# Performance work log

Measured on AMD Instinct MI355X. Metric: run time of the kernel, lower is better.

## Reference

```python
import jax, jax.numpy as jnp
import numpy as np

N, E = 10000, 160000
D, H, C, FF, L = 128, 4, 32, 512, 2
INNER = H * C
VOCAB, RELVOCAB = 32000, 100
EPS = 1e-6
GATE_BIAS = 3.0


def _layer_norm(x, w, b):
    mu = jnp.mean(x, axis=-1, keepdims=True)
    var = jnp.mean(jnp.square(x - mu), axis=-1, keepdims=True)
    return (x - mu) * jax.lax.rsqrt(var + EPS) * w + b


def setup_inputs() -> dict:
    key = jax.random.key(0)
    ks = jax.random.split(key, 24)
    s = 1.0 / np.sqrt(D)
    inp = {
        "node_ids": jax.random.randint(ks[0], (N,), 0, VOCAB),
        "edge_index": jax.random.randint(ks[1], (2, E), 0, N),
        "edge_ids": jax.random.randint(ks[2], (E,), 0, RELVOCAB),
        "node_emb": jax.random.normal(ks[3], (VOCAB, D), jnp.float32),
        "edge_emb": jax.random.normal(ks[4], (RELVOCAB, D), jnp.float32),
        # per-layer stacked params (torch Linear weight layout [out, in])
        "ln_w": jnp.ones((L, D), jnp.float32),
        "ln_b": jnp.zeros((L, D), jnp.float32),
        "q_w": jax.random.normal(ks[5], (L, INNER, D), jnp.float32) * (1.0 / np.sqrt(D * C)),
        "relA_w": jax.random.normal(ks[6], (L, FF, 2 * D), jnp.float32) * s,
        "relA_b": jnp.zeros((L, FF), jnp.float32),
        "relB_w": jax.random.normal(ks[7], (L, D, FF), jnp.float32) * s,
        "relB_b": jnp.zeros((L, D), jnp.float32),
        "relG_w": jax.random.normal(ks[8], (L, D, FF), jnp.float32) * s,
        "relG_b": jnp.zeros((L, D), jnp.float32),
        "k_w": jax.random.normal(ks[9], (L, INNER, 2 * D), jnp.float32) * s,
        "v_w": jax.random.normal(ks[10], (L, INNER, D), jnp.float32) * s,
        "o_w": jax.random.normal(ks[11], (L, D, INNER), jnp.float32) * (1.0 / np.sqrt(INNER)),
        "ff_ln_w": jnp.ones((L, D), jnp.float32),
        "ff_ln_b": jnp.zeros((L, D), jnp.float32),
        "wi_w": jax.random.normal(ks[12], (L, FF, D), jnp.float32) * s,
        "wo_w": jax.random.normal(ks[13], (L, D, FF), jnp.float32) * (1.0 / np.sqrt(FF)),
    }
    return inp


def _forward(node_ids, edge_index, edge_ids, node_emb, edge_emb, ln_w, ln_b,
             q_w, relA_w, relA_b, relB_w, relB_b, relG_w, relG_b,
             k_w, v_w, o_w, ff_ln_w, ff_ln_b, wi_w, wo_w):
    x = node_emb[node_ids]          # [N, D]
    ef = edge_emb[edge_ids]         # [E, D]
    src = edge_index[0]             # j (source / kv side)
    dst = edge_index[1]             # i (target / query side)
    for l in range(L):
        # --- relational self-attention ---
        q = _layer_norm(x, ln_w[l], ln_b[l])
        q = (q @ q_w[l].T).reshape(N, H, C)
        kv_j = x[src]                                   # [E, D]
        cat = jnp.concatenate([kv_j, ef], axis=-1)      # [E, 2D]
        inter = jax.nn.celu(cat @ relA_w[l].T + relA_b[l])   # [E, FF]
        gate = jax.nn.sigmoid(inter @ relG_w[l].T + relG_b[l] + GATE_BIAS)
        k_add = inter @ relB_w[l].T + relB_b[l]
        kv2 = kv_j * gate + k_add * (1.0 - gate)        # [E, D]
        k = (jnp.concatenate([kv2, ef], axis=-1) @ k_w[l].T).reshape(E, H, C)
        v = (kv2 @ v_w[l].T).reshape(E, H, C)
        scores = jnp.sum(q[dst] * k, axis=-1)           # [E, H]
        smax = jax.ops.segment_max(scores, dst, num_segments=N)
        ex = jnp.exp(scores - smax[dst])
        denom = jax.ops.segment_sum(ex, dst, num_segments=N)
        alpha = ex / denom[dst]                         # [E, H]
        msg = (v * alpha[..., None]).reshape(E, INNER)
        agg = jax.ops.segment_sum(msg, dst, num_segments=N)  # [N, INNER]
        x = x + agg @ o_w[l].T
        # --- feed-forward (T5-style, pre-LN, relu, residual) ---
        h = _layer_norm(x, ff_ln_w[l], ff_ln_b[l])
        x = x + jax.nn.relu(h @ wi_w[l].T) @ wo_w[l].T
    return x


def reference(node_ids, edge_index, edge_ids, node_emb, edge_emb, ln_w, ln_b,
              q_w, relA_w, relA_b, relB_w, relB_b, relG_w, relG_b,
              k_w, v_w, o_w, ff_ln_w, ff_ln_b, wi_w, wo_w):
    return _forward(node_ids, edge_index, edge_ids, node_emb, edge_emb, ln_w, ln_b,
                    q_w, relA_w, relA_b, relB_w, relB_b, relG_w, relG_b,
                    k_w, v_w, o_w, ff_ln_w, ff_ln_b, wi_w, wo_w)
```

## Files before the change

### kernel.cpp

```cpp
#include <hip/hip_runtime.h>
#include <hip/hip_bf16.h>

#define NN 10000
#define EE 160000
#define DD 128
#define HH 4
#define CC 32
#define FFF 512
#define LL 2
#define RELV 100
#define EPS 1e-6f
#define GATE_BIAS 3.0f
#define BM 64
#define NT 16

typedef __bf16 bf16x8 __attribute__((ext_vector_type(8)));
typedef float f32x4 __attribute__((ext_vector_type(4)));
typedef float f32x16 __attribute__((ext_vector_type(16)));

#define MFMA(a,b,c)   __builtin_amdgcn_mfma_f32_16x16x32_bf16((a),(b),(c),0,0,0)
#define MFMA32(a,b,c) __builtin_amdgcn_mfma_f32_32x32x16_bf16((a),(b),(c),0,0,0)

__device__ __forceinline__ int swzK(int e, int b){ return e*256 + (b ^ ((e&7)<<4)); }
__device__ __forceinline__ int swz128(int e, int b){ return e*256 + (b ^ ((e&7)<<4)); }
__device__ __forceinline__ int swz512(int e, int b){ return e*1024 + (b ^ ((e&7)<<4)); }

__global__ __launch_bounds__(128) void k_gx(
    const int* __restrict__ node_ids, const float* __restrict__ node_emb,
    float* __restrict__ x, ushort* __restrict__ xb, int* __restrict__ hist){
  int n = blockIdx.x, t = threadIdx.x;
  if (t == 0) hist[n] = 0;
  float v = node_emb[(long)node_ids[n]*DD + t];
  x[(long)n*DD + t] = v;
  __hip_bfloat16 h = __float2bfloat16(v);
  xb[(long)n*DD + t] = *(ushort*)&h;
}

__device__ __forceinline__ void wprep_one(
    const float* __restrict__ in, ushort* __restrict__ out, int tid, int IN, int instride){
  int lane = tid & 63;
  int grp  = tid >> 6;
  int nkb  = IN >> 4;
  int kb   = grp % nkb;
  int cb   = grp / nkb;
  int col  = cb*32 + (lane & 31);
  int k0   = kb*16 + (lane >> 5)*8;
  const float* p = in + (long)col*instride + k0;
  bf16x8 h;
  #pragma unroll
  for (int j=0;j<8;++j) h[j] = (__bf16)p[j];
  *(bf16x8*)(out + (long)tid*8) = h;
}

__global__ __launch_bounds__(256) void k_prep(
    const float* __restrict__ relG_w, const float* __restrict__ relB_w,
    const float* __restrict__ k_w, const float* __restrict__ v_w,
    const float* __restrict__ relA_w,
    ushort* __restrict__ Gwb, ushort* __restrict__ Bwb,
    ushort* __restrict__ Kwb, ushort* __restrict__ Vwb, ushort* __restrict__ A1b){
  int tid = blockIdx.x*256 + threadIdx.x;
  if (tid < DD*FFF/8){
    wprep_one(relG_w, Gwb, tid, FFF, FFF);
    wprep_one(relB_w, Bwb, tid, FFF, FFF);
  }
  if (tid < DD*DD/8){
    wprep_one(k_w, Kwb, tid, DD, 256);
    wprep_one(v_w, Vwb, tid, DD, DD);
  }
  {
    int o = tid / DD, i = tid % DD;
    __hip_bfloat16 h = __float2bfloat16(relA_w[(long)o*256 + i]);
    A1b[tid] = *(ushort*)&h;
  }
}

__global__ __launch_bounds__(256) void k_f2b4(
    const float* __restrict__ q_w, const float* __restrict__ o_w,
    const float* __restrict__ wi_w, const float* __restrict__ wo_w,
    ushort* __restrict__ Qwb, ushort* __restrict__ Owb,
    ushort* __restrict__ Wib, ushort* __restrict__ Wob){
  long i = (long)blockIdx.x*256 + threadIdx.x;
  const long nV = (long)LL*DD*DD;
  if (i < nV){
    __hip_bfloat16 h1 = __float2bfloat16(q_w[i]); Qwb[i] = *(ushort*)&h1;
    __hip_bfloat16 h2 = __float2bfloat16(o_w[i]); Owb[i] = *(ushort*)&h2;
  }
  {
    __hip_bfloat16 h3 = __float2bfloat16(wi_w[i]); Wib[i] = *(ushort*)&h3;
    __hip_bfloat16 h4 = __float2bfloat16(wo_w[i]); Wob[i] = *(ushort*)&h4;
  }
}

__global__ __launch_bounds__(256) void k_ea(
    const float* __restrict__ edge_emb, const float* __restrict__ relA_w,
    const float* __restrict__ relA_b, const float* __restrict__ k_w,
    ushort* __restrict__ EA2b, float* __restrict__ EKf){
  int rel = blockIdx.x, t = threadIdx.x;
  __shared__ float emb[128];
  if (t < 128) emb[t] = edge_emb[(long)rel*DD + t];
  __syncthreads();
  for (int f=t; f<FFF; f+=256){
    const float* wr = relA_w + (long)f*256 + 128;
    float s = relA_b[f];
    for (int i=0;i<128;++i) s += emb[i]*wr[i];
    __hip_bfloat16 h = __float2bfloat16(s);
    EA2b[(long)rel*FFF + f] = *(ushort*)&h;
  }
  if (t < 128){
    const float* wr = k_w + (long)t*256 + 128;
    float s = 0.f;
    for (int i=0;i<128;++i) s += emb[i]*wr[i];
    EKf[(long)rel*DD + t] = s;
  }
}

__global__ __launch_bounds__(256) void k_hist(const int* __restrict__ dst, int* __restrict__ hist){
  int e = blockIdx.x*256 + threadIdx.x;
  if (e < EE) atomicAdd(&hist[dst[e]], 1);
}
__global__ __launch_bounds__(256) void k_scan(const int* __restrict__ hist, int* __restrict__ cursor){
  __shared__ int tsum[256];
  const int t = threadIdx.x;
  const int PER = (NN + 255) / 256;
  const int base = t*PER;
  int s = 0;
  for (int i=0;i<PER;++i){ int idx = base+i; if (idx < NN) s += hist[idx]; }
  tsum[t] = s;
  __syncthreads();
  if (t == 0){
    int run = 0;
    for (int i=0;i<256;++i){ int v = tsum[i]; tsum[i] = run; run += v; }
  }
  __syncthreads();
  int run = tsum[t];
  for (int i=0;i<PER;++i){
    int idx = base+i;
    if (idx < NN){ int v = hist[idx]; cursor[idx] = run; run += v; }
  }
}
__global__ __launch_bounds__(256) void k_scatter(const int* __restrict__ dst,
    int* __restrict__ cursor, int* __restrict__ perm){
  int e = blockIdx.x*256 + threadIdx.x;
  if (e < EE){
    int p = atomicAdd(&cursor[dst[e]], 1);
    perm[p] = e;
  }
}

__global__ __launch_bounds__(256) void k_lnq_xa(
    const float* __restrict__ x, const float* __restrict__ lnw, const float* __restrict__ lnb,
    const ushort* __restrict__ qwb, const ushort* __restrict__ a1b,
    float* __restrict__ q, ushort* __restrict__ XAb,
    float* __restrict__ agg, float* __restrict__ denom){
  __shared__ __align__(16) unsigned char HB[NT*256];
  __shared__ __align__(16) unsigned char HR[NT*256];
  const int n0 = blockIdx.x*NT;
  const int t = threadIdx.x;
  const int e = t>>4, s = t&15;
  const int w = t>>6, l = t&63, lr = l&15, lg = l>>4;
  {
    float4 z4 = {0.f,0.f,0.f,0.f};
    float* ap = agg + (long)n0*DD + t*8;
    *(float4*)ap = z4; *(float4*)(ap+4) = z4;
    if (t < NT*HH) denom[n0*HH + t] = 0.f;
  }
  {
    const float* xp = x + (long)(n0+e)*DD + s*8;
    float xv[8];
    *(float4*)&xv[0] = *(const float4*)xp;
    *(float4*)&xv[4] = *(const float4*)(xp+4);
    float sm = 0.f;
    #pragma unroll
    for (int i=0;i<8;++i) sm += xv[i];
    sm += __shfl_xor(sm,1); sm += __shfl_xor(sm,2);
    sm += __shfl_xor(sm,4); sm += __shfl_xor(sm,8);
    float mu = sm*(1.f/DD);
    float sq = 0.f;
    #pragma unroll
    for (int i=0;i<8;++i){ float d = xv[i]-mu; sq += d*d; }
    sq += __shfl_xor(sq,1); sq += __shfl_xor(sq,2);
    sq += __shfl_xor(sq,4); sq += __shfl_xor(sq,8);
    float rstd = rsqrtf(sq*(1.f/DD) + EPS);
    float4 w0 = *(const float4*)(lnw + s*8), w1 = *(const float4*)(lnw + s*8 + 4);
    float4 b0 = *(const float4*)(lnb + s*8), b1 = *(const float4*)(lnb + s*8 + 4);
    float wv[8] = {w0.x,w0.y,w0.z,w0.w,w1.x,w1.y,w1.z,w1.w};
    float bv[8] = {b0.x,b0.y,b0.z,b0.w,b1.x,b1.y,b1.z,b1.w};
    bf16x8 hb, hr;
    #pragma unroll
    for (int i=0;i<8;++i){
      hb[i] = (__bf16)((xv[i]-mu)*rstd*wv[i] + bv[i]);
      hr[i] = (__bf16)xv[i];
    }
    *(bf16x8*)(HB + swz128(e, s*16)) = hb;
    *(bf16x8*)(HR + swz128(e, s*16)) = hr;
  }
  __syncthreads();
  {
    const int o0 = w*32;
    f32x4 z = {0.f,0.f,0.f,0.f};
    f32x4 acc[2] = {z,z};
    #pragma unroll
    for (int k4=0;k4<4;++k4){
      bf16x8 a = *(const bf16x8*)(HB + swz128(lr, k4*64 + lg*16));
      #pragma unroll
      for (int nt=0;nt<2;++nt){
        bf16x8 b = *(const bf16x8*)(qwb + (long)(o0+nt*16+lr)*128 + k4*32 + lg*8);
        acc[nt] = MFMA(a, b, acc[nt]);
      }
    }
    #pragma unroll
    for (int nt=0;nt<2;++nt)
      #pragma unroll
      for (int r=0;r<4;++r)
        q[(long)(n0 + lg*4 + r)*DD + o0 + nt*16 + lr] = acc[nt][r];
  }
  {
    const int f0w = w*128;
    f32x4 z = {0.f,0.f,0.f,0.f};
    f32x4 acc[8] = {z,z,z,z,z,z,z,z};
    #pragma unroll
    for (int k4=0;k4<4;++k4){
      bf16x8 a = *(const bf16x8*)(HR + swz128(lr, k4*64 + lg*16));
      #pragma unroll
      for (int nt=0;nt<8;++nt){
        bf16x8 b = *(const bf16x8*)(a1b + (long)(f0w+nt*16+lr)*128 + k4*32 + lg*8);
        acc[nt] = MFMA(a, b, acc[nt]);
      }
    }
    #pragma unroll
    for (int nt=0;nt<8;++nt)
      #pragma unroll
      for (int r=0;r<4;++r){
        __hip_bfloat16 h = __float2bfloat16(acc[nt][r]);
        XAb[(long)(n0+lg*4+r)*FFF + f0w+nt*16+lr] = *(ushort*)&h;
      }
  }
}

__global__ __launch_bounds__(512,4) void k_edge(
    const ushort* __restrict__ xb, const ushort* __restrict__ XAb,
    const ushort* __restrict__ EAb, const float* __restrict__ EKf,
    const float* __restrict__ q,
    const int* __restrict__ src, const int* __restrict__ dst, const int* __restrict__ eids,
    const int* __restrict__ perm,
    const ushort* __restrict__ Gwb, const float* __restrict__ Gb,
    const ushort* __restrict__ Bwb, const float* __restrict__ Bb,
    const ushort* __restrict__ Kwb, const ushort* __restrict__ Vwb,
    float* __restrict__ agg, float* __restrict__ denom)
{
  __shared__ __align__(16) unsigned char KVB[BM*256];
  __shared__ __align__(16) unsigned char INTB[2][BM*256];
  __shared__ float EXL[BM][HH];
  __shared__ int srcl[BM], dstl[BM], eidl[BM];

  const int e0 = blockIdx.x * BM;
  const int t  = threadIdx.x;
  const int w  = t >> 6;
  const int l  = t & 63;
  const int c32 = l & 31;
  const int hi  = l >> 5;
  const int R = w >> 2;
  const int C = w & 3;
  const int oc = C*32 + c32;

  if (t < BM){
    int pe = perm[e0+t];
    srcl[t] = src[pe]; dstl[t] = dst[pe]; eidl[t] = eids[pe];
  }
  __syncthreads();

  {
    const uint4* xbu = (const uint4*)xb;
    #pragma unroll
    for (int it=0; it<2; ++it){
      int g = it*512 + t;
      int e = g >> 4, qq = g & 15;
      *(uint4*)(KVB + swzK(e, qq*16)) = xbu[(long)srcl[e]*16 + qq];
    }
  }

  f32x16 gbG, gbB;
  {
    float bg = Gb[oc] + GATE_BIAS;
    float bb = Bb[oc];
    #pragma unroll
    for (int i=0;i<16;++i){ gbG[i] = bg; gbB[i] = bb; }
  }

  bf16x8 xa8[2], ea8[2];
  #pragma unroll
  for (int it=0; it<2; ++it){
    int g = it*512 + t;
    int e = g >> 4, c8 = g & 15;
    xa8[it] = *(const bf16x8*)(XAb + (long)srcl[e]*FFF + c8*8);
    ea8[it] = *(const bf16x8*)(EAb + (long)eidl[e]*FFF + c8*8);
  }

  #pragma unroll
  for (int ch=0; ch<4; ++ch){
    bf16x8 o[2];
    #pragma unroll
    for (int it=0; it<2; ++it){
      #pragma unroll
      for (int j=0;j<8;++j){
        float s = (float)xa8[it][j] + (float)ea8[it][j];
        o[it][j] = (__bf16)((s > 0.f) ? s : (__expf(s) - 1.f));
      }
    }
    unsigned char* INTp = INTB[ch & 1];
    #pragma unroll
    for (int it=0; it<2; ++it){
      int g = it*512 + t;
      int e = g >> 4, c8 = g & 15;
      *(bf16x8*)(INTp + swzK(e, c8*16)) = o[it];
    }
    __syncthreads();
    if (ch < 3){
      #pragma unroll
      for (int it=0; it<2; ++it){
        int g = it*512 + t;
        int e = g >> 4, c8 = g & 15;
        xa8[it] = *(const bf16x8*)(XAb + (long)srcl[e]*FFF + (ch+1)*128 + c8*8);
        ea8[it] = *(const bf16x8*)(EAb + (long)eidl[e]*FFF + (ch+1)*128 + c8*8);
      }
    }
    bf16x8 af[8];
    #pragma unroll
    for (int i=0;i<8;++i) af[i] = *(const bf16x8*)(INTp + swzK(R*32 + c32, i*32 + hi*16));
    {
      const ushort* Wg = Gwb + ((long)(C*32 + ch*8)*64 + l)*8;
      bf16x8 wf[8];
      #pragma unroll
      for (int i=0;i<8;++i) wf[i] = *(const bf16x8*)(Wg + (long)i*512);
      #pragma unroll
      for (int i=0;i<8;++i) gbG = MFMA32(af[i], wf[i], gbG);
    }
    {
      const ushort* Wb = Bwb + ((long)(C*32 + ch*8)*64 + l)*8;
      bf16x8 wf[8];
      #pragma unroll
      for (int i=0;i<8;++i) wf[i] = *(const bf16x8*)(Wb + (long)i*512);
      #pragma unroll
      for (int i=0;i<8;++i) gbB = MFMA32(af[i], wf[i], gbB);
    }
  }

  #pragma unroll
  for (int r=0;r<16;++r){
    int row = (r&3) + 8*(r>>2) + 4*hi;
    int gr = R*32 + row;
    float g  = 1.f/(1.f + __expf(-gbG[r]));
    float kv = (float)*(const __bf16*)(KVB + swzK(gr, oc*2));
    float k2 = gbB[r] + g*(kv - gbB[r]);
    *(__bf16*)(KVB + swzK(gr, oc*2)) = (__bf16)k2;
  }
  __syncthreads();

  f32x16 ka, va;
  #pragma unroll
  for (int i=0;i<16;++i){ ka[i] = 0.f; va[i] = 0.f; }
  {
    bf16x8 af[8];
    #pragma unroll
    for (int i=0;i<8;++i) af[i] = *(const bf16x8*)(KVB + swzK(R*32 + c32, i*32 + hi*16));
    {
      const ushort* Wk = Kwb + ((long)(C*8)*64 + l)*8;
      bf16x8 wf[8];
      #pragma unroll
      for (int i=0;i<8;++i) wf[i] = *(const bf16x8*)(Wk + (long)i*512);
      #pragma unroll
      for (int i=0;i<8;++i) ka = MFMA32(af[i], wf[i], ka);
    }
    {
      const ushort* Wv = Vwb + ((long)(C*8)*64 + l)*8;
      bf16x8 wf[8];
      #pragma unroll
      for (int i=0;i<8;++i) wf[i] = *(const bf16x8*)(Wv + (long)i*512);
      #pragma unroll
      for (int i=0;i<8;++i) va = MFMA32(af[i], wf[i], va);
    }
  }
  __syncthreads();

  #pragma unroll
  for (int r=0;r<16;++r){
    int row = (r&3) + 8*(r>>2) + 4*hi;
    int gr = R*32 + row;
    unsigned char* ab = (gr < 32) ? KVB : INTB[0];
    *(float*)(ab + ((gr & 31)*128 + oc)*4) = va[r];
  }
  #pragma unroll
  for (int r=0;r<16;++r){
    int row = (r&3) + 8*(r>>2) + 4*hi;
    int gr = R*32 + row;
    int dn = dstl[gr];
    float kv = ka[r] + EKf[(long)eidl[gr]*DD + oc];
    float p = kv * q[(long)dn*DD + oc];
    p += __shfl_xor(p, 1); p += __shfl_xor(p, 2);
    p += __shfl_xor(p, 4); p += __shfl_xor(p, 8);
    p += __shfl_xor(p, 16);
    if (c32 == 0) EXL[gr][C] = __expf(p);
  }
  __syncthreads();

  {
    const int col = t & 127;
    const int rg  = t >> 7;
    const int r0  = rg*16;
    const int h   = col >> 5;
    const unsigned char* ab = (rg < 2) ? KVB : INTB[0];
    const int rb = (rg & 1) * 16;
    float acc = 0.f;
    int cur = dstl[r0];
    for (int r=0; r<16; ++r){
      int dn = dstl[r0+r];
      if (dn != cur){
        atomicAdd(&agg[(long)cur*DD + col], acc);
        acc = 0.f; cur = dn;
      }
      acc += *(const float*)(ab + ((rb + r)*128 + col)*4) * EXL[r0+r][h];
    }
    atomicAdd(&agg[(long)cur*DD + col], acc);
    if (col < HH){
      float da = 0.f; int cur2 = dstl[r0];
      for (int r=r0; r<r0+16; ++r){
        int dn = dstl[r];
        if (dn != cur2){
          atomicAdd(&denom[cur2*HH + col], da);
          da = 0.f; cur2 = dn;
        }
        da += EXL[r][col];
      }
      atomicAdd(&denom[cur2*HH + col], da);
    }
  }
}

__global__ __launch_bounds__(256) void k_node(
    const float* __restrict__ agg, const float* __restrict__ denom,
    const ushort* __restrict__ owb,
    const float* __restrict__ lnw, const float* __restrict__ lnb,
    const ushort* __restrict__ wib, const ushort* __restrict__ wob,
    float* __restrict__ x, ushort* __restrict__ xb){
  __shared__ __align__(16) unsigned char AB[NT*256];
  __shared__ __align__(16) unsigned char IB[NT*1024];
  __shared__ __align__(16) float XO[NT][132];
  const int n0 = blockIdx.x*NT;
  const int t = threadIdx.x;
  const int e = t>>4, s = t&15;
  const int w = t>>6, l = t&63, lr = l&15, lg = l>>4;

  {
    const float* ap = agg + (long)(n0+e)*DD + s*8;
    float av[8];
    *(float4*)&av[0] = *(const float4*)ap;
    *(float4*)&av[4] = *(const float4*)(ap+4);
    float dinv = 1.f / denom[(n0+e)*HH + (s>>2)];
    bf16x8 hb;
    #pragma unroll
    for (int i=0;i<8;++i) hb[i] = (__bf16)(av[i]*dinv);
    *(bf16x8*)(AB + swz128(e, s*16)) = hb;
  }
  __syncthreads();

  {
    const int o0 = w*32;
    f32x4 z = {0.f,0.f,0.f,0.f};
    f32x4 acc[2] = {z,z};
    #pragma unroll
    for (int k4=0;k4<4;++k4){
      bf16x8 a = *(const bf16x8*)(AB + swz128(lr, k4*64 + lg*16));
      #pragma unroll
      for (int nt=0;nt<2;++nt){
        bf16x8 b = *(const bf16x8*)(owb + (long)(o0+nt*16+lr)*128 + k4*32 + lg*8);
        acc[nt] = MFMA(a, b, acc[nt]);
      }
    }
    #pragma unroll
    for (int nt=0;nt<2;++nt)
      #pragma unroll
      for (int r=0;r<4;++r)
        XO[lg*4+r][o0+nt*16+lr] = acc[nt][r];
  }
  __syncthreads();

  float x1[8];
  {
    const float* xp = x + (long)(n0+e)*DD + s*8;
    float xv[8];
    *(float4*)&xv[0] = *(const float4*)xp;
    *(float4*)&xv[4] = *(const float4*)(xp+4);
    #pragma unroll
    for (int i=0;i<8;++i) x1[i] = xv[i] + XO[e][s*8+i];
    float sm = 0.f;
    #pragma unroll
    for (int i=0;i<8;++i) sm += x1[i];
    sm += __shfl_xor(sm,1); sm += __shfl_xor(sm,2);
    sm += __shfl_xor(sm,4); sm += __shfl_xor(sm,8);
    float mu = sm*(1.f/DD);
    float sq = 0.f;
    #pragma unroll
    for (int i=0;i<8;++i){ float d = x1[i]-mu; sq += d*d; }
    sq += __shfl_xor(sq,1); sq += __shfl_xor(sq,2);
    sq += __shfl_xor(sq,4); sq += __shfl_xor(sq,8);
    float rstd = rsqrtf(sq*(1.f/DD) + EPS);
    float4 w0 = *(const float4*)(lnw + s*8), w1 = *(const float4*)(lnw + s*8 + 4);
    float4 b0 = *(const float4*)(lnb + s*8), b1 = *(const float4*)(lnb + s*8 + 4);
    float wv[8] = {w0.x,w0.y,w0.z,w0.w,w1.x,w1.y,w1.z,w1.w};
    float bv[8] = {b0.x,b0.y,b0.z,b0.w,b1.x,b1.y,b1.z,b1.w};
    bf16x8 hb;
    #pragma unroll
    for (int i=0;i<8;++i) hb[i] = (__bf16)((x1[i]-mu)*rstd*wv[i] + bv[i]);
    __syncthreads();
    *(bf16x8*)(AB + swz128(e, s*16)) = hb;
  }
  __syncthreads();

  {
    const int f0w = w*128;
    f32x4 z = {0.f,0.f,0.f,0.f};
    f32x4 acc[8] = {z,z,z,z,z,z,z,z};
    #pragma unroll
    for (int k4=0;k4<4;++k4){
      bf16x8 a = *(const bf16x8*)(AB + swz128(lr, k4*64 + lg*16));
      #pragma unroll
      for (int nt=0;nt<8;++nt){
        bf16x8 b = *(const bf16x8*)(wib + (long)(f0w+nt*16+lr)*128 + k4*32 + lg*8);
        acc[nt] = MFMA(a, b, acc[nt]);
      }
    }
    #pragma unroll
    for (int nt=0;nt<8;++nt)
      #pragma unroll
      for (int r=0;r<4;++r){
        int e2 = lg*4 + r;
        int f = f0w + nt*16 + lr;
        float va = acc[nt][r];
        *(__bf16*)(IB + swz512(e2, f*2)) = (__bf16)fmaxf(va, 0.f);
      }
  }
  __syncthreads();

  {
    const int o0 = w*32;
    f32x4 z = {0.f,0.f,0.f,0.f};
    f32x4 acc[2] = {z,z};
    #pragma unroll
    for (int k16=0;k16<16;++k16){
      bf16x8 a = *(const bf16x8*)(IB + swz512(lr, k16*64 + lg*16));
      #pragma unroll
      for (int nt=0;nt<2;++nt){
        bf16x8 b = *(const bf16x8*)(wob + (long)(o0+nt*16+lr)*512 + k16*32 + lg*8);
        acc[nt] = MFMA(a, b, acc[nt]);
      }
    }
    #pragma unroll
    for (int nt=0;nt<2;++nt)
      #pragma unroll
      for (int r=0;r<4;++r)
        XO[lg*4+r][o0+nt*16+lr] = acc[nt][r];
  }
  __syncthreads();

  {
    float xn[8];
    #pragma unroll
    for (int i=0;i<8;++i) xn[i] = x1[i] + XO[e][s*8+i];
    float* xp = x + (long)(n0+e)*DD + s*8;
    *(float4*)xp = *(float4*)&xn[0];
    *(float4*)(xp+4) = *(float4*)&xn[4];
    bf16x8 hb;
    #pragma unroll
    for (int i=0;i<8;++i) hb[i] = (__bf16)xn[i];
    *(bf16x8*)(xb + (long)(n0+e)*DD + s*8) = hb;
  }
}

extern "C" void kernel_launch(void* const* d_in, const int* in_sizes, int n_in,
                              void* d_out, int out_size, void* d_ws, size_t ws_size,
                              hipStream_t stream) {
  const int* node_ids   = (const int*)d_in[0];
  const int* edge_index = (const int*)d_in[1];
  const int* edge_ids   = (const int*)d_in[2];
  const float* node_emb = (const float*)d_in[3];
  const float* edge_emb = (const float*)d_in[4];
  const float* ln_w   = (const float*)d_in[5];
  const float* ln_b   = (const float*)d_in[6];
  const float* q_w    = (const float*)d_in[7];
  const float* relA_w = (const float*)d_in[8];
  const float* relA_b = (const float*)d_in[9];
  const float* relB_w = (const float*)d_in[10];
  const float* relB_b = (const float*)d_in[11];
  const float* relG_w = (const float*)d_in[12];
  const float* relG_b = (const float*)d_in[13];
  const float* k_w    = (const float*)d_in[14];
  const float* v_w    = (const float*)d_in[15];
  const float* o_w    = (const float*)d_in[16];
  const float* ff_ln_w= (const float*)d_in[17];
  const float* ff_ln_b= (const float*)d_in[18];
  const float* wi_w   = (const float*)d_in[19];
  const float* wo_w   = (const float*)d_in[20];
  const int* src = edge_index;
  const int* dst = edge_index + EE;

  float* ws = (float*)d_ws;
  float* x   = ws;  ws += (long)NN*DD;
  float* q   = ws;  ws += (long)NN*DD;
  float* denom = ws; ws += NN*HH;
  float* agg   = ws; ws += (long)NN*DD;
  float* EKf   = ws; ws += (long)LL*RELV*DD;
  int* hist   = (int*)ws; ws += NN;
  int* perm   = (int*)ws; ws += EE;
  ushort* xb  = (ushort*)ws; ws += (long)NN*DD/2;
  ushort* XAb = (ushort*)ws; ws += (long)NN*FFF/2;
  ushort* EAb = (ushort*)ws; ws += (long)LL*RELV*FFF/2;
  ushort* A1b = (ushort*)ws; ws += (long)LL*FFF*DD/2;
  ushort* Gwb = (ushort*)ws; ws += (long)LL*DD*FFF/2;
  ushort* Bwb = (ushort*)ws; ws += (long)LL*DD*FFF/2;
  ushort* Kwb = (ushort*)ws; ws += (long)LL*DD*DD/2;
  ushort* Vwb = (ushort*)ws; ws += (long)LL*DD*DD/2;
  ushort* Qwb = (ushort*)ws; ws += (long)LL*DD*DD/2;
  ushort* Owb = (ushort*)ws; ws += (long)LL*DD*DD/2;
  ushort* Wib = (ushort*)ws; ws += (long)LL*FFF*DD/2;
  ushort* Wob = (ushort*)ws; ws += (long)LL*DD*FFF/2;

  k_gx<<<NN, 128, 0, stream>>>(node_ids, node_emb, x, xb, hist);
  k_hist<<<(EE+255)/256, 256, 0, stream>>>(dst, hist);
  k_scan<<<1, 256, 0, stream>>>(hist, hist);
  k_scatter<<<(EE+255)/256, 256, 0, stream>>>(dst, hist, perm);
  for (int l=0; l<LL; ++l){
    k_prep<<<256, 256, 0, stream>>>(
        relG_w + (long)l*DD*FFF, relB_w + (long)l*DD*FFF,
        k_w + (long)l*DD*256,    v_w + (long)l*DD*DD,
        relA_w + (long)l*FFF*256,
        Gwb + (long)l*DD*FFF, Bwb + (long)l*DD*FFF,
        Kwb + (long)l*DD*DD,  Vwb + (long)l*DD*DD, A1b + (long)l*FFF*DD);
    k_ea<<<RELV, 256, 0, stream>>>(edge_emb, relA_w + (long)l*FFF*256, relA_b + (long)l*FFF,
                                   k_w + (long)l*DD*256, EAb + (long)l*RELV*FFF, EKf + (long)l*RELV*DD);
  }
  k_f2b4<<<512, 256, 0, stream>>>(q_w, o_w, wi_w, wo_w, Qwb, Owb, Wib, Wob);

  for (int l=0; l<LL; ++l){
    k_lnq_xa<<<NN/NT, 256, 0, stream>>>(x, ln_w + l*DD, ln_b + l*DD,
        Qwb + (long)l*DD*DD, A1b + (long)l*FFF*DD, q, XAb, agg, denom);
    k_edge<<<EE/BM, 512, 0, stream>>>(xb, XAb, EAb + (long)l*RELV*FFF, EKf + (long)l*RELV*DD,
        q, src, dst, edge_ids, perm,
        Gwb + (long)l*DD*FFF,  relG_b + (long)l*DD,
        Bwb + (long)l*DD*FFF,  relB_b + (long)l*DD,
        Kwb + (long)l*DD*DD,   Vwb + (long)l*DD*DD,
        agg, denom);
    k_node<<<NN/NT, 256, 0, stream>>>(agg, denom, Owb + (long)l*DD*DD,
        ff_ln_w + l*DD, ff_ln_b + l*DD,
        Wib + (long)l*FFF*DD, Wob + (long)l*DD*FFF, x, xb);
  }
  hipMemcpyAsync(d_out, x, (size_t)NN*DD*sizeof(float), hipMemcpyDeviceToDevice, stream);
}
```

Measured before the change: 443.2 us.

## Fuse histogram into gather kernel and cut k_edge register pressure for occupancy

The standalone histogram kernel is folded into the embedding-gather kernel, which now handles two nodes per block, and the histogram is zeroed with a memset instead. In k_edge, the eight A-fragments are no longer held in registers across the G/B and K/V MFMA loops. They are reloaded from LDS in halves of four, and the launch bound rises from 4 to 6 waves per SIMD. This trades more LDS reads for lower VGPR use and higher occupancy, and risks spills or LDS-bandwidth stalls.

```diff
diff --git a/kernel.cpp b/kernel.cpp
--- a/kernel.cpp
+++ b/kernel.cpp
@@ -25,15 +25,21 @@
 __device__ __forceinline__ int swz128(int e, int b){ return e*256 + (b ^ ((e&7)<<4)); }
 __device__ __forceinline__ int swz512(int e, int b){ return e*1024 + (b ^ ((e&7)<<4)); }
 
-__global__ __launch_bounds__(128) void k_gx(
+__global__ __launch_bounds__(256) void k_gx(
     const int* __restrict__ node_ids, const float* __restrict__ node_emb,
-    float* __restrict__ x, ushort* __restrict__ xb, int* __restrict__ hist){
-  int n = blockIdx.x, t = threadIdx.x;
-  if (t == 0) hist[n] = 0;
-  float v = node_emb[(long)node_ids[n]*DD + t];
-  x[(long)n*DD + t] = v;
+    float* __restrict__ x, ushort* __restrict__ xb,
+    const int* __restrict__ dst, int* __restrict__ hist){
+  int b = blockIdx.x, t = threadIdx.x;
+  int n = b*2 + (t>>7);
+  int c = t & 127;
+  float v = node_emb[(long)node_ids[n]*DD + c];
+  x[(long)n*DD + c] = v;
   __hip_bfloat16 h = __float2bfloat16(v);
-  xb[(long)n*DD + t] = *(ushort*)&h;
+  xb[(long)n*DD + c] = *(ushort*)&h;
+  if (t < 32){
+    int e = b*32 + t;
+    atomicAdd(&hist[dst[e]], 1);
+  }
 }
 
 __device__ __forceinline__ void wprep_one(
@@ -114,10 +120,6 @@
   }
 }
 
-__global__ __launch_bounds__(256) void k_hist(const int* __restrict__ dst, int* __restrict__ hist){
-  int e = blockIdx.x*256 + threadIdx.x;
-  if (e < EE) atomicAdd(&hist[dst[e]], 1);
-}
 __global__ __launch_bounds__(256) void k_scan(const int* __restrict__ hist, int* __restrict__ cursor){
   __shared__ int tsum[256];
   const int t = threadIdx.x;
@@ -237,7 +239,7 @@
   }
 }
 
-__global__ __launch_bounds__(512,4) void k_edge(
+__global__ __launch_bounds__(512,6) void k_edge(
     const ushort* __restrict__ xb, const ushort* __restrict__ XAb,
     const ushort* __restrict__ EAb, const float* __restrict__ EKf,
     const float* __restrict__ q,
@@ -324,24 +326,33 @@
         ea8[it] = *(const bf16x8*)(EAb + (long)eidl[e]*FFF + (ch+1)*128 + c8*8);
       }
     }
-    bf16x8 af[8];
-    #pragma unroll
-    for (int i=0;i<8;++i) af[i] = *(const bf16x8*)(INTp + swzK(R*32 + c32, i*32 + hi*16));
     {
       const ushort* Wg = Gwb + ((long)(C*32 + ch*8)*64 + l)*8;
-      bf16x8 wf[8];
-      #pragma unroll
-      for (int i=0;i<8;++i) wf[i] = *(const bf16x8*)(Wg + (long)i*512);
-      #pragma unroll
-      for (int i=0;i<8;++i) gbG = MFMA32(af[i], wf[i], gbG);
+      #pragma unroll
+      for (int h2=0; h2<2; ++h2){
+        bf16x8 wf[4];
+        #pragma unroll
+        for (int i=0;i<4;++i) wf[i] = *(const bf16x8*)(Wg + (long)(h2*4+i)*512);
+        #pragma unroll
+        for (int i=0;i<4;++i){
+          bf16x8 a = *(const bf16x8*)(INTp + swzK(R*32 + c32, (h2*4+i)*32 + hi*16));
+          gbG = MFMA32(a, wf[i], gbG);
+        }
+      }
     }
     {
       const ushort* Wb = Bwb + ((long)(C*32 + ch*8)*64 + l)*8;
-      bf16x8 wf[8];
-      #pragma unroll
-      for (int i=0;i<8;++i) wf[i] = *(const bf16x8*)(Wb + (long)i*512);
-      #pragma unroll
-      for (int i=0;i<8;++i) gbB = MFMA32(af[i], wf[i], gbB);
+      #pragma unroll
+      for (int h2=0; h2<2; ++h2){
+        bf16x8 wf[4];
+        #pragma unroll
+        for (int i=0;i<4;++i) wf[i] = *(const bf16x8*)(Wb + (long)(h2*4+i)*512);
+        #pragma unroll
+        for (int i=0;i<4;++i){
+          bf16x8 a = *(const bf16x8*)(INTp + swzK(R*32 + c32, (h2*4+i)*32 + hi*16));
+          gbB = MFMA32(a, wf[i], gbB);
+        }
+      }
     }
   }
 
@@ -360,24 +371,31 @@
   #pragma unroll
   for (int i=0;i<16;++i){ ka[i] = 0.f; va[i] = 0.f; }
   {
-    bf16x8 af[8];
-    #pragma unroll
-    for (int i=0;i<8;++i) af[i] = *(const bf16x8*)(KVB + swzK(R*32 + c32, i*32 + hi*16));
-    {
-      const ushort* Wk = Kwb + ((long)(C*8)*64 + l)*8;
-      bf16x8 wf[8];
-      #pragma unroll
-      for (int i=0;i<8;++i) wf[i] = *(const bf16x8*)(Wk + (long)i*512);
-      #pragma unroll
-      for (int i=0;i<8;++i) ka = MFMA32(af[i], wf[i], ka);
-    }
-    {
-      const ushort* Wv = Vwb + ((long)(C*8)*64 + l)*8;
-      bf16x8 wf[8];
-      #pragma unroll
-      for (int i=0;i<8;++i) wf[i] = *(const bf16x8*)(Wv + (long)i*512);
-      #pragma unroll
-      for (int i=0;i<8;++i) va = MFMA32(af[i], wf[i], va);
+    const ushort* Wk = Kwb + ((long)(C*8)*64 + l)*8;
+    #pragma unroll
+    for (int h2=0; h2<2; ++h2){
+      bf16x8 wf[4];
+      #pragma unroll
+      for (int i=0;i<4;++i) wf[i] = *(const bf16x8*)(Wk + (long)(h2*4+i)*512);
+      #pragma unroll
+      for (int i=0;i<4;++i){
+        bf16x8 a = *(const bf16x8*)(KVB + swzK(R*32 + c32, (h2*4+i)*32 + hi*16));
+        ka = MFMA32(a, wf[i], ka);
+      }
+    }
+  }
+  {
+    const ushort* Wv = Vwb + ((long)(C*8)*64 + l)*8;
+    #pragma unroll
+    for (int h2=0; h2<2; ++h2){
+      bf16x8 wf[4];
+      #pragma unroll
+      for (int i=0;i<4;++i) wf[i] = *(const bf16x8*)(Wv + (long)(h2*4+i)*512);
+      #pragma unroll
+      for (int i=0;i<4;++i){
+        bf16x8 a = *(const bf16x8*)(KVB + swzK(R*32 + c32, (h2*4+i)*32 + hi*16));
+        va = MFMA32(a, wf[i], va);
+      }
     }
   }
   __syncthreads();
@@ -624,8 +642,8 @@
   ushort* Wib = (ushort*)ws; ws += (long)LL*FFF*DD/2;
   ushort* Wob = (ushort*)ws; ws += (long)LL*DD*FFF/2;
 
-  k_gx<<<NN, 128, 0, stream>>>(node_ids, node_emb, x, xb, hist);
-  k_hist<<<(EE+255)/256, 256, 0, stream>>>(dst, hist);
+  hipMemsetAsync(hist, 0, NN*sizeof(int), stream);
+  k_gx<<<NN/2, 256, 0, stream>>>(node_ids, node_emb, x, xb, dst, hist);
   k_scan<<<1, 256, 0, stream>>>(hist, hist);
   k_scatter<<<(EE+255)/256, 256, 0, stream>>>(dst, hist, perm);
   for (int l=0; l<LL; ++l){
```

Measured after the change: 499.7 us. 12.7% more time.
